# Kernel tuning notes

Hardware: AMD Instinct MI355X
Metric: run time of the kernel (lower is better)

Reference implementation:

```python
import jax, jax.numpy as jnp
import numpy as np

V, H = 30522, 768
B, S = 64, 512
NEW_ROWS = 10004          # 1 pad + num_labels(10000) + depth(2) + 1
N_NODES = NEW_ROWS - 2    # rows [1:-1] of new_embedding go through the graph
N_SOFT = 8
N_EDGES = 50000
LEAKY_SLOPE = 0.2


def setup_inputs() -> dict:
    key = jax.random.key(0)
    ks = jax.random.split(key, 8)
    x = jax.random.randint(ks[0], (B, S), 0, V + NEW_ROWS - 1, dtype=jnp.int64)
    edge_index = jax.random.randint(ks[1], (2, N_EDGES), 0, N_NODES, dtype=jnp.int64)
    original_weight = jax.random.normal(ks[2], (V, H), jnp.float32) * 0.02
    new_weight = jax.random.normal(ks[3], (NEW_ROWS, H), jnp.float32) * 0.02
    new_weight = new_weight.at[0].set(0.0)  # padding row prepended in __init__
    soft_prompt_weight = jax.random.normal(ks[4], (N_SOFT, H), jnp.float32) * 0.02
    W_gat = jax.random.normal(ks[5], (H, H), jnp.float32) / np.sqrt(H)
    a_src = jax.random.normal(ks[6], (H,), jnp.float32) * 0.05
    a_dst = jax.random.normal(ks[7], (H,), jnp.float32) * 0.05
    return {"x": x, "edge_index": edge_index, "original_weight": original_weight,
            "new_weight": new_weight, "soft_prompt_weight": soft_prompt_weight,
            "W_gat": W_gat, "a_src": a_src, "a_dst": a_dst}


def _gat_layer(feat, W_gat, a_src, a_dst, edge_index):
    """Single-head GAT over label graph: gather-attend-scatter. feat: [N, H]."""
    n = feat.shape[0]
    h = feat @ W_gat                                   # [N, H]
    src, dst = edge_index[0], edge_index[1]            # [E], [E]
    s_src = h @ a_src                                  # [N]
    s_dst = h @ a_dst                                  # [N]
    e = jax.nn.leaky_relu(s_src[src] + s_dst[dst], LEAKY_SLOPE)   # [E]
    # segment softmax over incoming edges of each dst node
    m = jax.ops.segment_max(e, dst, num_segments=n)
    ex = jnp.exp(e - m[dst])
    denom = jax.ops.segment_sum(ex, dst, num_segments=n)
    alpha = ex / (denom[dst] + 1e-16)                  # [E]
    agg = jax.ops.segment_sum(alpha[:, None] * h[src], dst, num_segments=n)  # [N, H]
    return feat + agg                                  # residual connection


def _combined_weight(original_weight, new_weight, W_gat, a_src, a_dst, edge_index):
    edge_features = new_weight[1:-1]                   # [N_NODES, H]
    edge_features = _gat_layer(edge_features, W_gat, a_src, a_dst, edge_index)
    edge_features = jnp.concatenate([edge_features, new_weight[-1:]], axis=0)
    return jnp.concatenate([original_weight, edge_features], axis=0)  # [V+NEW_ROWS-1, H]


def reference(x, edge_index, original_weight, new_weight, soft_prompt_weight,
              W_gat, a_src, a_dst):
    bsz = x.shape[0]
    weight = _combined_weight(original_weight, new_weight, W_gat, a_src, a_dst, edge_index)
    other_emb = weight[x[:, N_SOFT:]]                  # [B, S-N_SOFT, H] big gather
    soft = jnp.broadcast_to(soft_prompt_weight[None], (bsz, N_SOFT, H))
    return jnp.concatenate([soft, other_emb], axis=1)  # [B, S, H]
```

## Files before the change

kernel.cpp:

```cpp
#include <hip/hip_runtime.h>
#include <stdint.h>

#define HDIM  768
#define VOCAB 30522
#define NNODE 10002
#define NEDGE 50000
#define NROWS 10004
#define SLOPE 0.2f
#define CAP   32
#define RCAP  32
#define NROWT 32768

constexpr size_t OFF_H    = 0;
constexpr size_t SZ_HB    = (size_t)NNODE * HDIM * 2;
constexpr size_t OFF_FB   = OFF_H + SZ_HB;
constexpr size_t OFF_WT   = OFF_FB + SZ_HB;
constexpr size_t OFF_WAS  = OFF_WT + (size_t)HDIM * HDIM * 2;
constexpr size_t OFF_WAD  = OFF_WAS + HDIM * 4;
constexpr size_t SZ_N4    = 40032;
constexpr size_t OFF_SS   = OFF_WAD + HDIM * 4;
constexpr size_t OFF_SD   = OFF_SS + SZ_N4;
constexpr size_t OFF_CNT  = OFF_SD + SZ_N4;
constexpr size_t OFF_NCT  = OFF_CNT + SZ_N4;
constexpr size_t OFF_SLOT = OFF_NCT + SZ_N4;
constexpr size_t OFF_NL   = OFF_SLOT + (size_t)NNODE * CAP * 2;
constexpr int    ZERO_CNT = 10008 + 10008;

__device__ __forceinline__ unsigned short f2bf(float f) {
  unsigned int u = __float_as_uint(f);
  u += 0x7FFFu + ((u >> 16) & 1u);
  return (unsigned short)(u >> 16);
}
__device__ __forceinline__ float bf2f(unsigned short b) {
  return __uint_as_float(((unsigned int)b) << 16);
}

typedef __attribute__((ext_vector_type(8))) short bf16x8;
typedef __attribute__((ext_vector_type(4))) float f32x4;

__device__ __forceinline__ void gl2lds16(const unsigned short* g, unsigned short* l) {
  __builtin_amdgcn_global_load_lds(
      (const __attribute__((address_space(1))) unsigned int*)g,
      (__attribute__((address_space(3))) unsigned int*)l, 16, 0, 0);
}

__device__ __forceinline__ void fma12(float* acc, float ex,
                                      const unsigned short* hr, int lane) {
  const ushort4* p = (const ushort4*)(hr + lane * 12);
  ushort4 u0 = p[0], u1 = p[1], u2 = p[2];
  acc[0] += ex * bf2f(u0.x); acc[1]  += ex * bf2f(u0.y);
  acc[2] += ex * bf2f(u0.z); acc[3]  += ex * bf2f(u0.w);
  acc[4] += ex * bf2f(u1.x); acc[5]  += ex * bf2f(u1.y);
  acc[6] += ex * bf2f(u1.z); acc[7]  += ex * bf2f(u1.w);
  acc[8] += ex * bf2f(u2.x); acc[9]  += ex * bf2f(u2.y);
  acc[10]+= ex * bf2f(u2.z); acc[11] += ex * bf2f(u2.w);
}

__global__ __launch_bounds__(256) void k_pre(const float* __restrict__ W,
                                             const float* __restrict__ a_s,
                                             const float* __restrict__ a_d,
                                             float* __restrict__ wa_s,
                                             float* __restrict__ wa_d,
                                             int* __restrict__ count) {
  int bid = blockIdx.x, tid = threadIdx.x;
  if (bid >= 192) {
    int i = (bid - 192) * 256 + tid;
    if (i < ZERO_CNT) count[i] = 0;
    return;
  }
  int lane = tid & 63, wv = tid >> 6;
  int row = bid * 4 + wv;
  float ss = 0.f, sd = 0.f;
  for (int n = lane; n < HDIM; n += 64) {
    float w = W[(size_t)row * HDIM + n];
    ss += w * a_s[n];
    sd += w * a_d[n];
  }
#pragma unroll
  for (int off = 32; off; off >>= 1) {
    ss += __shfl_down(ss, off, 64);
    sd += __shfl_down(sd, off, 64);
  }
  if (lane == 0) { wa_s[row] = ss; wa_d[row] = sd; }
}

__global__ __launch_bounds__(256) void k_stage1(const float* __restrict__ feat,
                                                const float* __restrict__ wa_s,
                                                const float* __restrict__ wa_d,
                                                const float* __restrict__ W,
                                                const int* __restrict__ ei,
                                                unsigned short* __restrict__ featbf,
                                                float* __restrict__ s_s,
                                                float* __restrict__ s_d,
                                                unsigned short* __restrict__ wT,
                                                int* __restrict__ count,
                                                unsigned short* __restrict__ slots) {
  int bid = blockIdx.x, tid = threadIdx.x;
  if (bid < 2501) {
    int lane = tid & 63, wv = tid >> 6;
    int r = bid * 4 + wv;
    if (r >= NNODE) return;
    const float4* fr = (const float4*)(feat + (size_t)r * HDIM);
    ushort4* ob = (ushort4*)(featbf + (size_t)r * HDIM);
    float ss = 0.f, sd = 0.f;
#pragma unroll
    for (int i = 0; i < 3; ++i) {
      int c = lane + i * 64;
      float4 v = fr[c];
      float4 vs = ((const float4*)wa_s)[c];
      float4 vd = ((const float4*)wa_d)[c];
      ss += v.x * vs.x + v.y * vs.y + v.z * vs.z + v.w * vs.w;
      sd += v.x * vd.x + v.y * vd.y + v.z * vd.z + v.w * vd.w;
      ushort4 o;
      o.x = f2bf(v.x); o.y = f2bf(v.y); o.z = f2bf(v.z); o.w = f2bf(v.w);
      ob[c] = o;
    }
#pragma unroll
    for (int off = 32; off; off >>= 1) {
      ss += __shfl_down(ss, off, 64);
      sd += __shfl_down(sd, off, 64);
    }
    if (lane == 0) { s_s[r] = ss; s_d[r] = sd; }
    return;
  }
  if (bid < 3077) {
    __shared__ float tile[32][33];
    int b2 = bid - 2501;
    int tx0 = (b2 % 24) * 32, ty0 = (b2 / 24) * 32;
    int cx = tid & 31, cy = tid >> 5;
#pragma unroll
    for (int r = 0; r < 4; ++r)
      tile[cy + r * 8][cx] = W[(size_t)(ty0 + cy + r * 8) * HDIM + tx0 + cx];
    __syncthreads();
#pragma unroll
    for (int r = 0; r < 4; ++r)
      wT[(size_t)(tx0 + cy + r * 8) * HDIM + ty0 + cx] = f2bf(tile[cx][cy + r * 8]);
    return;
  }
  int e = (bid - 3077) * 256 + tid;
  if (e < NEDGE) {
    int src = ei[e], dst = ei[NEDGE + e];
    int pos = atomicAdd(count + dst, 1);
    if (pos < CAP) slots[dst * CAP + pos] = (unsigned short)src;
  }
}

__global__ __launch_bounds__(256) void k_stage2(const unsigned short* __restrict__ A,
                                                const unsigned short* __restrict__ BT,
                                                unsigned short* __restrict__ Hout,
                                                const int* __restrict__ x,
                                                const float* __restrict__ orig,
                                                const float* __restrict__ nw,
                                                const float* __restrict__ soft,
                                                int* __restrict__ nct,
                                                int* __restrict__ nlist,
                                                float* __restrict__ out) {
  int bid = blockIdx.x, tid = threadIdx.x;
  int lane = tid & 63, wv = tid >> 6;
  if (bid % 10 != 0) {
    int gather_id = bid - bid / 10 - 1;
    if (gather_id >= 8192) return;
    int row = gather_id * 4 + wv;
    int s = row & 511;
    const float* src;
    if (s < 8) {
      src = soft + (size_t)s * HDIM;
    } else {
      int idx = x[row];
      if (idx >= VOCAB && idx < VOCAB + NNODE) {
        if (lane == 0) {
          int node = idx - VOCAB;
          int p = atomicAdd(nct + node, 1);
          if (p < RCAP) nlist[node * RCAP + p] = row;
        }
        return;
      }
      src = (idx < VOCAB) ? orig + (size_t)idx * HDIM
                          : nw + (size_t)(NROWS - 1) * HDIM;
    }
    const uint4* s4 = (const uint4*)src;
    uint4* d4 = (uint4*)(out + (size_t)row * HDIM);
    d4[lane]       = s4[lane];
    d4[lane + 64]  = s4[lane + 64];
    d4[lane + 128] = s4[lane + 128];
    return;
  }
  int b = bid / 10;
  __shared__ __align__(16) unsigned short As[64 * 32];
  __shared__ __align__(16) unsigned short Bs[128 * 32];
  int m0 = (b % 157) * 64, n0 = (b / 157) * 128;
  int q = lane >> 4, lr = lane & 15;

  f32x4 acc[4][2];
#pragma unroll
  for (int i = 0; i < 4; ++i)
#pragma unroll
    for (int j = 0; j < 2; ++j) acc[i][j] = 0.f;

  for (int kt = 0; kt < 24; ++kt) {
    int k0 = kt * 32;
    {
      int row = tid >> 2, kk = (tid & 3) << 3;
      int grow = m0 + row;
      grow = grow <= NNODE - 1 ? grow : NNODE - 1;
      gl2lds16(A + (size_t)grow * HDIM + k0 + kk, As + (size_t)wv * 512);
    }
#pragma unroll
    for (int t = 0; t < 2; ++t) {
      int c = wv * 128 + t * 64 + lane;
      int row = c >> 2, kk = (c & 3) << 3;
      gl2lds16(BT + (size_t)(n0 + row) * HDIM + k0 + kk, Bs + (size_t)wv * 1024 + t * 512);
    }
    __syncthreads();
    bf16x8 a[4], bb[2];
#pragma unroll
    for (int i = 0; i < 4; ++i)
      a[i] = *(const bf16x8*)(As + (i * 16 + lr) * 32 + q * 8);
#pragma unroll
    for (int j = 0; j < 2; ++j)
      bb[j] = *(const bf16x8*)(Bs + (wv * 32 + j * 16 + lr) * 32 + q * 8);
#pragma unroll
    for (int i = 0; i < 4; ++i)
#pragma unroll
      for (int j = 0; j < 2; ++j)
        acc[i][j] = __builtin_amdgcn_mfma_f32_16x16x32_bf16(a[i], bb[j], acc[i][j], 0, 0, 0);
    __syncthreads();
  }
#pragma unroll
  for (int i = 0; i < 4; ++i) {
    int mbase = m0 + i * 16 + q * 4;
#pragma unroll
    for (int j = 0; j < 2; ++j) {
      int n = n0 + wv * 32 + j * 16 + lr;
#pragma unroll
      for (int rg = 0; rg < 4; ++rg) {
        int m = mbase + rg;
        if (m < NNODE) Hout[(size_t)m * HDIM + n] = f2bf(acc[i][j][rg]);
      }
    }
  }
}

__global__ __launch_bounds__(256) void k_aggregate(const int* __restrict__ count,
                                                   const unsigned short* __restrict__ slots,
                                                   const float* __restrict__ s_s,
                                                   const float* __restrict__ s_d,
                                                   const unsigned short* __restrict__ h,
                                                   const float* __restrict__ feat,
                                                   const int* __restrict__ nct,
                                                   const int* __restrict__ nlist,
                                                   float* __restrict__ out) {
  int lane = threadIdx.x & 63, wv = threadIdx.x >> 6;
  int n = blockIdx.x * 4 + wv;
  if (n >= NNODE) return;
  int rows = nct[n];
  if (rows == 0) return;
  rows = rows < RCAP ? rows : RCAP;
  int deg = count[n]; deg = deg < CAP ? deg : CAP;
  const unsigned short* sl = slots + n * CAP;
  float sdn = s_d[n];
  float mx = -3.4e38f;
  for (int e = 0; e < deg; ++e) {
    float v = s_s[sl[e]] + sdn;
    v = v > 0.f ? v : SLOPE * v;
    mx = fmaxf(mx, v);
  }
  float den = 0.f;
  float acc[12];
#pragma unroll
  for (int j = 0; j < 12; ++j) acc[j] = 0.f;
  int e = 0;
  for (; e + 1 < deg; e += 2) {
    int s0 = sl[e], s1 = sl[e + 1];
    float v0 = s_s[s0] + sdn; v0 = v0 > 0.f ? v0 : SLOPE * v0;
    float v1 = s_s[s1] + sdn; v1 = v1 > 0.f ? v1 : SLOPE * v1;
    float ex0 = __expf(v0 - mx), ex1 = __expf(v1 - mx);
    den += ex0 + ex1;
    fma12(acc, ex0, h + (size_t)s0 * HDIM, lane);
    fma12(acc, ex1, h + (size_t)s1 * HDIM, lane);
  }
  if (e < deg) {
    int s0 = sl[e];
    float v0 = s_s[s0] + sdn; v0 = v0 > 0.f ? v0 : SLOPE * v0;
    float ex0 = __expf(v0 - mx);
    den += ex0;
    fma12(acc, ex0, h + (size_t)s0 * HDIM, lane);
  }
  float inv = 1.f / (den + 1e-16f);
  const float4* fr = (const float4*)(feat + (size_t)n * HDIM + lane * 12);
  float4 f0 = fr[0], f1 = fr[1], f2 = fr[2];
  f0.x += acc[0] * inv;  f0.y += acc[1] * inv;
  f0.z += acc[2] * inv;  f0.w += acc[3] * inv;
  f1.x += acc[4] * inv;  f1.y += acc[5] * inv;
  f1.z += acc[6] * inv;  f1.w += acc[7] * inv;
  f2.x += acc[8] * inv;  f2.y += acc[9] * inv;
  f2.z += acc[10] * inv; f2.w += acc[11] * inv;
  for (int ri = 0; ri < rows; ++ri) {
    int r = nlist[n * RCAP + ri];
    float4* d = (float4*)(out + (size_t)r * HDIM + lane * 12);
    d[0] = f0; d[1] = f1; d[2] = f2;
  }
}

extern "C" void kernel_launch(void* const* d_in, const int* in_sizes, int n_in,
                              void* d_out, int out_size, void* d_ws, size_t ws_size,
                              hipStream_t stream) {
  const int* x    = (const int*)d_in[0];
  const int* ei   = (const int*)d_in[1];
  const float* og = (const float*)d_in[2];
  const float* nw = (const float*)d_in[3];
  const float* sp = (const float*)d_in[4];
  const float* W  = (const float*)d_in[5];
  const float* as = (const float*)d_in[6];
  const float* ad = (const float*)d_in[7];
  const float* feat = nw + HDIM;

  char* ws = (char*)d_ws;
  unsigned short* hbuf   = (unsigned short*)(ws + OFF_H);
  unsigned short* featbf = (unsigned short*)(ws + OFF_FB);
  unsigned short* wT     = (unsigned short*)(ws + OFF_WT);
  float* wa_s            = (float*)(ws + OFF_WAS);
  float* wa_d            = (float*)(ws + OFF_WAD);
  float* s_s             = (float*)(ws + OFF_SS);
  float* s_d             = (float*)(ws + OFF_SD);
  int* count             = (int*)(ws + OFF_CNT);
  int* nct               = (int*)(ws + OFF_NCT);
  unsigned short* slots  = (unsigned short*)(ws + OFF_SLOT);
  int* nlist             = (int*)(ws + OFF_NL);
  float* out             = (float*)d_out;

  k_pre<<<272, 256, 0, stream>>>(W, as, ad, wa_s, wa_d, count);
  k_stage1<<<3273, 256, 0, stream>>>(feat, wa_s, wa_d, W, ei,
                                     featbf, s_s, s_d, wT, count, slots);
  k_stage2<<<9420, 256, 0, stream>>>(featbf, wT, hbuf, x, og, nw, sp,
                                     nct, nlist, out);
  k_aggregate<<<(NNODE + 3) / 4, 256, 0, stream>>>(count, slots, s_s, s_d,
                                                   hbuf, feat, nct, nlist, out);
}
```

Before: 291.8 us.

## Split fused gather/GEMM kernel and use K=64 tiles with XOR-swizzled LDS

Splits the mixed kernel, which interleaved gather blocks with GEMM blocks, into a separate gather kernel and a dedicated GEMM kernel. The GEMM now loads K=64 slices per iteration, which halves the number of barrier-separated iterations. LDS addresses are XOR-swizzled to avoid bank conflicts on the wider rows. The gather and GEMM no longer overlap within one launch, and the split adds an extra launch.

```diff
diff --git a/kernel.cpp b/kernel.cpp
--- a/kernel.cpp
+++ b/kernel.cpp
@@ -9,7 +9,6 @@
 #define SLOPE 0.2f
 #define CAP   32
 #define RCAP  32
-#define NROWT 32768
 
 constexpr size_t OFF_H    = 0;
 constexpr size_t SZ_HB    = (size_t)NNODE * HDIM * 2;
@@ -145,49 +144,46 @@
   }
 }
 
-__global__ __launch_bounds__(256) void k_stage2(const unsigned short* __restrict__ A,
-                                                const unsigned short* __restrict__ BT,
-                                                unsigned short* __restrict__ Hout,
-                                                const int* __restrict__ x,
-                                                const float* __restrict__ orig,
-                                                const float* __restrict__ nw,
-                                                const float* __restrict__ soft,
-                                                int* __restrict__ nct,
-                                                int* __restrict__ nlist,
-                                                float* __restrict__ out) {
-  int bid = blockIdx.x, tid = threadIdx.x;
-  int lane = tid & 63, wv = tid >> 6;
-  if (bid % 10 != 0) {
-    int gather_id = bid - bid / 10 - 1;
-    if (gather_id >= 8192) return;
-    int row = gather_id * 4 + wv;
-    int s = row & 511;
-    const float* src;
-    if (s < 8) {
-      src = soft + (size_t)s * HDIM;
-    } else {
-      int idx = x[row];
-      if (idx >= VOCAB && idx < VOCAB + NNODE) {
-        if (lane == 0) {
-          int node = idx - VOCAB;
-          int p = atomicAdd(nct + node, 1);
-          if (p < RCAP) nlist[node * RCAP + p] = row;
-        }
-        return;
+__global__ __launch_bounds__(256) void k_gatherA(const int* __restrict__ x,
+                                                 const float* __restrict__ orig,
+                                                 const float* __restrict__ nw,
+                                                 const float* __restrict__ soft,
+                                                 int* __restrict__ nct,
+                                                 int* __restrict__ nlist,
+                                                 float* __restrict__ out) {
+  int lane = threadIdx.x & 63, wv = threadIdx.x >> 6;
+  int row = blockIdx.x * 4 + wv;
+  int s = row & 511;
+  const float* src;
+  if (s < 8) {
+    src = soft + (size_t)s * HDIM;
+  } else {
+    int idx = x[row];
+    if (idx >= VOCAB && idx < VOCAB + NNODE) {
+      if (lane == 0) {
+        int node = idx - VOCAB;
+        int p = atomicAdd(nct + node, 1);
+        if (p < RCAP) nlist[node * RCAP + p] = row;
       }
-      src = (idx < VOCAB) ? orig + (size_t)idx * HDIM
-                          : nw + (size_t)(NROWS - 1) * HDIM;
-    }
-    const uint4* s4 = (const uint4*)src;
-    uint4* d4 = (uint4*)(out + (size_t)row * HDIM);
-    d4[lane]       = s4[lane];
-    d4[lane + 64]  = s4[lane + 64];
-    d4[lane + 128] = s4[lane + 128];
-    return;
-  }
-  int b = bid / 10;
-  __shared__ __align__(16) unsigned short As[64 * 32];
-  __shared__ __align__(16) unsigned short Bs[128 * 32];
+      return;
+    }
+    src = (idx < VOCAB) ? orig + (size_t)idx * HDIM
+                        : nw + (size_t)(NROWS - 1) * HDIM;
+  }
+  const uint4* s4 = (const uint4*)src;
+  uint4* d4 = (uint4*)(out + (size_t)row * HDIM);
+  d4[lane]       = s4[lane];
+  d4[lane + 64]  = s4[lane + 64];
+  d4[lane + 128] = s4[lane + 128];
+}
+
+__global__ __launch_bounds__(256) void k_gemm(const unsigned short* __restrict__ A,
+                                              const unsigned short* __restrict__ BT,
+                                              unsigned short* __restrict__ Hout) {
+  __shared__ __align__(16) unsigned short As[64 * 64];
+  __shared__ __align__(16) unsigned short Bs[128 * 64];
+  int b = blockIdx.x;
+  int tid = threadIdx.x, lane = tid & 63, wv = tid >> 6;
   int m0 = (b % 157) * 64, n0 = (b / 157) * 128;
   int q = lane >> 4, lr = lane & 15;
 
@@ -197,33 +193,43 @@
 #pragma unroll
     for (int j = 0; j < 2; ++j) acc[i][j] = 0.f;
 
-  for (int kt = 0; kt < 24; ++kt) {
-    int k0 = kt * 32;
-    {
-      int row = tid >> 2, kk = (tid & 3) << 3;
+  for (int kt = 0; kt < 12; ++kt) {
+    int k0 = kt * 64;
+#pragma unroll
+    for (int t = 0; t < 2; ++t) {
+      int c = wv * 128 + t * 64 + lane;
+      int row = c >> 3;
+      int kk = (((c & 7) ^ (row & 7)) << 3);
       int grow = m0 + row;
       grow = grow <= NNODE - 1 ? grow : NNODE - 1;
-      gl2lds16(A + (size_t)grow * HDIM + k0 + kk, As + (size_t)wv * 512);
-    }
-#pragma unroll
-    for (int t = 0; t < 2; ++t) {
-      int c = wv * 128 + t * 64 + lane;
-      int row = c >> 2, kk = (c & 3) << 3;
-      gl2lds16(BT + (size_t)(n0 + row) * HDIM + k0 + kk, Bs + (size_t)wv * 1024 + t * 512);
+      gl2lds16(A + (size_t)grow * HDIM + k0 + kk,
+               As + (size_t)(wv * 128 + t * 64) * 8);
+    }
+#pragma unroll
+    for (int t = 0; t < 4; ++t) {
+      int c = wv * 256 + t * 64 + lane;
+      int row = c >> 3;
+      int kk = (((c & 7) ^ (row & 7)) << 3);
+      gl2lds16(BT + (size_t)(n0 + row) * HDIM + k0 + kk,
+               Bs + (size_t)(wv * 256 + t * 64) * 8);
     }
     __syncthreads();
-    bf16x8 a[4], bb[2];
-#pragma unroll
-    for (int i = 0; i < 4; ++i)
-      a[i] = *(const bf16x8*)(As + (i * 16 + lr) * 32 + q * 8);
-#pragma unroll
-    for (int j = 0; j < 2; ++j)
-      bb[j] = *(const bf16x8*)(Bs + (wv * 32 + j * 16 + lr) * 32 + q * 8);
-#pragma unroll
-    for (int i = 0; i < 4; ++i)
+#pragma unroll
+    for (int ks = 0; ks < 2; ++ks) {
+      bf16x8 a[4], bb[2];
+      int base = ((ks << 5) | (q << 3)) ^ ((lr & 7) << 3);
+#pragma unroll
+      for (int i = 0; i < 4; ++i)
+        a[i] = *(const bf16x8*)(As + (i * 16 + lr) * 64 + base);
 #pragma unroll
       for (int j = 0; j < 2; ++j)
-        acc[i][j] = __builtin_amdgcn_mfma_f32_16x16x32_bf16(a[i], bb[j], acc[i][j], 0, 0, 0);
+        bb[j] = *(const bf16x8*)(Bs + (wv * 32 + j * 16 + lr) * 64 + base);
+#pragma unroll
+      for (int i = 0; i < 4; ++i)
+#pragma unroll
+        for (int j = 0; j < 2; ++j)
+          acc[i][j] = __builtin_amdgcn_mfma_f32_16x16x32_bf16(a[i], bb[j], acc[i][j], 0, 0, 0);
+    }
     __syncthreads();
   }
 #pragma unroll
@@ -332,8 +338,8 @@
   k_pre<<<272, 256, 0, stream>>>(W, as, ad, wa_s, wa_d, count);
   k_stage1<<<3273, 256, 0, stream>>>(feat, wa_s, wa_d, W, ei,
                                      featbf, s_s, s_d, wT, count, slots);
-  k_stage2<<<9420, 256, 0, stream>>>(featbf, wT, hbuf, x, og, nw, sp,
-                                     nct, nlist, out);
+  k_gatherA<<<8192, 256, 0, stream>>>(x, og, nw, sp, nct, nlist, out);
+  k_gemm<<<942, 256, 0, stream>>>(featbf, wT, hbuf);
   k_aggregate<<<(NNODE + 3) / 4, 256, 0, stream>>>(count, slots, s_s, s_d,
                                                    hbuf, feat, nct, nlist, out);
 }
```

Measured after the change: 261.5 us. -10.4%, faster.
